# Optimization experiments

Hardware: AMD Instinct MI355X
Metric: run time of the kernel (lower is better)

The kernel has to match this reference:

```python
import jax, jax.numpy as jnp
import numpy as np

N = 100_000      # nodes
E = 1_600_000    # edges
DIN = 128
DH = 128
DOUT = 2
BN_EPS = 1e-5


def setup_inputs() -> dict:
    key = jax.random.key(0)
    ks = jax.random.split(key, 14)
    s_in = 1.0 / np.sqrt(DIN)
    s_h = 1.0 / np.sqrt(DH)
    return {
        "x": jax.random.normal(ks[0], (N, DIN), jnp.float32),
        "edge_index": jax.random.randint(ks[1], (2, E), 0, N, jnp.int32),
        "W1": jax.random.normal(ks[2], (DIN, DH), jnp.float32) * s_in,
        "b1": jnp.zeros((DH,), jnp.float32),
        "W2": jax.random.normal(ks[3], (DH, DH), jnp.float32) * s_h,
        "b2": jnp.zeros((DH,), jnp.float32),
        "W3": jax.random.normal(ks[4], (DH, DH), jnp.float32) * s_h,
        "b3": jnp.zeros((DH,), jnp.float32),
        "gamma": jnp.ones((DH,), jnp.float32),
        "beta": jnp.zeros((DH,), jnp.float32),
        "Wc": jax.random.normal(ks[5], (DH, DH), jnp.float32) * s_h,
        "bc": jnp.zeros((DH,), jnp.float32),
        "Wr": jax.random.normal(ks[6], (DH, DOUT), jnp.float32) * s_h,
        "br": jnp.zeros((DOUT,), jnp.float32),
    }


def reference(x, edge_index, W1, b1, W2, b2, W3, b3, gamma, beta, Wc, bc, Wr, br):
    src, dst = edge_index[0], edge_index[1]
    # GCN symmetric normalization with self-loops (deg includes self-loop)
    deg = jnp.zeros((N,), x.dtype).at[dst].add(1.0) + 1.0
    dinv = jax.lax.rsqrt(deg)
    coef = (dinv[src] * dinv[dst])[:, None]        # [E,1]
    self_coef = (dinv * dinv)[:, None]             # [N,1] self-loop weight

    def gcn_conv(h, W, b):
        h = h @ W                                  # [N,DH] dense transform
        agg = jnp.zeros((N, h.shape[1]), h.dtype).at[dst].add(h[src] * coef)
        return agg + h * self_coef + b

    h = jax.nn.relu(gcn_conv(x, W1, b1))
    h = jax.nn.relu(gcn_conv(h, W2, b2))   # dropout is identity at inference
    h = jax.nn.relu(gcn_conv(h, W3, b3))
    # BatchNorm1d over the node dimension (training-mode batch statistics)
    mu = h.mean(axis=0)
    var = h.var(axis=0)
    h = (h - mu) * jax.lax.rsqrt(var + BN_EPS) * gamma + beta
    h = jax.nn.relu(h @ Wc + bc)
    return h @ Wr + br
```

## Files before the change

### kernel.cpp

```cpp
#include <hip/hip_runtime.h>

#define DHC 128
#define BSHIFT 8
#define BSIZE 256

typedef __attribute__((ext_vector_type(8))) __bf16 bf16x8;
typedef __attribute__((ext_vector_type(8))) unsigned short ushort8;
typedef __attribute__((ext_vector_type(4))) float floatx4;

__device__ inline unsigned short f2bf(float f) {
    unsigned int u = __float_as_uint(f);
    return (unsigned short)((u + 0x7FFFu + ((u >> 16) & 1u)) >> 16);
}
__device__ inline float bf2f_lo(unsigned int v) { return __uint_as_float(v << 16); }
__device__ inline float bf2f_hi(unsigned int v) { return __uint_as_float(v & 0xFFFF0000u); }


__global__ __launch_bounds__(256) void bucket_hist(const int* __restrict__ dst,
                                                   int* __restrict__ bcount, int e) {
    __shared__ int h[512];
    for (int i = threadIdx.x; i < 512; i += 256) h[i] = 0;
    __syncthreads();
    int base = blockIdx.x * 4096 + threadIdx.x;
#pragma unroll
    for (int j = 0; j < 16; j++) {
        int i = base + j * 256;
        if (i < e) atomicAdd(&h[dst[i] >> BSHIFT], 1);
    }
    __syncthreads();
    for (int i = threadIdx.x; i < 512; i += 256)
        if (h[i]) atomicAdd(&bcount[i], h[i]);
}

__global__ void bucket_scan(const int* __restrict__ bcount, int* __restrict__ bbase,
                            int* __restrict__ bcur, int* __restrict__ row_ptr,
                            int nb, int n, int e) {
    __shared__ int s[512];
    int t = threadIdx.x;
    s[t] = (t < nb) ? bcount[t] : 0;
    __syncthreads();
    for (int off = 1; off < 512; off <<= 1) {
        int add = (t >= off) ? s[t - off] : 0;
        __syncthreads();
        s[t] += add;
        __syncthreads();
    }
    if (t < nb) {
        int ex = (t == 0) ? 0 : s[t - 1];
        bbase[t] = ex;
        bcur[t] = ex;
    }
    if (t == 0) {
        bbase[nb] = e;
        row_ptr[n] = e;
    }
}

__global__ __launch_bounds__(256) void bucket_scatter(const int* __restrict__ src,
                                                      const int* __restrict__ dst,
                                                      int* __restrict__ bcur,
                                                      int2* __restrict__ ebuf, int e) {
    __shared__ int h[512];
    __shared__ int rsv[512];
    for (int i = threadIdx.x; i < 512; i += 256) h[i] = 0;
    __syncthreads();
    int base = blockIdx.x * 4096 + threadIdx.x;
    int sreg[16], dreg[16];
#pragma unroll
    for (int j = 0; j < 16; j++) {
        int i = base + j * 256;
        if (i < e) {
            sreg[j] = src[i];
            dreg[j] = dst[i];
            atomicAdd(&h[dreg[j] >> BSHIFT], 1);
        } else {
            dreg[j] = -1;
        }
    }
    __syncthreads();
    for (int i = threadIdx.x; i < 512; i += 256) {
        int c = h[i];
        rsv[i] = c ? atomicAdd(&bcur[i], c) : 0;
        h[i] = 0;
    }
    __syncthreads();
#pragma unroll
    for (int j = 0; j < 16; j++) {
        if (dreg[j] >= 0) {
            int b = dreg[j] >> BSHIFT;
            int pos = rsv[b] + atomicAdd(&h[b], 1);
            ebuf[pos] = make_int2(sreg[j], dreg[j]);
        }
    }
}

__global__ __launch_bounds__(256) void bucket_build(const int2* __restrict__ ebuf,
                                                    const int* __restrict__ bbase,
                                                    int* __restrict__ row_ptr,
                                                    int* __restrict__ csr_src,
                                                    float* __restrict__ dinv,
                                                    float* __restrict__ selfc, int n) {
    __shared__ int ldeg[256];
    __shared__ int lcur[256];
    int b = blockIdx.x;
    int d0 = b << BSHIFT;
    int t = threadIdx.x;
    int beg = bbase[b], end = bbase[b + 1];
    ldeg[t] = 0;
    __syncthreads();
    for (int i = beg + t; i < end; i += 256) atomicAdd(&ldeg[ebuf[i].y - d0], 1);
    __syncthreads();
    int deg = ldeg[t];
    lcur[t] = deg;
    __syncthreads();
    for (int off = 1; off < 256; off <<= 1) {
        int add = (t >= off) ? lcur[t - off] : 0;
        __syncthreads();
        lcur[t] += add;
        __syncthreads();
    }
    int rp = beg + lcur[t] - deg;
    int node = d0 + t;
    if (node < n) {
        row_ptr[node] = rp;
        float dv = rsqrtf((float)(deg + 1));
        dinv[node] = dv;
        selfc[node] = dv * dv;
    }
    __syncthreads();
    lcur[t] = rp;
    __syncthreads();
    for (int i = beg + t; i < end; i += 256) {
        int2 p = ebuf[i];
        int pos = atomicAdd(&lcur[p.y - d0], 1);
        csr_src[pos] = p.x;
    }
}

__global__ void wconv_k(const float* __restrict__ W, unsigned short* __restrict__ WT) {
    int i = blockIdx.x * 256 + threadIdx.x;
    int nn = i >> 7, k = i & 127;
    WT[i] = f2bf(W[k * 128 + nn]);
}

template <int MODE, int AF32>
__global__ __launch_bounds__(256) void gemm_k(const void* __restrict__ Avoid,
                                              const unsigned short* __restrict__ WT,
                                              const float* __restrict__ bias,
                                              unsigned short* __restrict__ outB,
                                              float* __restrict__ outF,
                                              const float* __restrict__ Wr,
                                              const float* __restrict__ br, int n) {
    __shared__ unsigned short Ws[32 * 512];
    {
        for (int c = threadIdx.x; c < 2048; c += 256) {
            int f = c >> 6;
            int l = c & 63;
            int ks = f >> 3, ct = f & 7;
            int nn = ct * 16 + (l & 15);
            int kb = ks * 32 + (l >> 4) * 8;
            *(uint4*)(&Ws[c * 8]) = *(const uint4*)(&WT[nn * 128 + kb]);
        }
    }
    __syncthreads();
    const int wave = threadIdx.x >> 6;
    const int lane = threadIdx.x & 63;
    const int rowbase = blockIdx.x * 128 + wave * 32;
    const int m = lane & 15;
    const int kq = lane >> 4;

    floatx4 acc[2][8];
#pragma unroll
    for (int rt = 0; rt < 2; rt++)
#pragma unroll
        for (int ct = 0; ct < 8; ct++) acc[rt][ct] = (floatx4){0.f, 0.f, 0.f, 0.f};

    const int r0 = min(rowbase + m, n - 1);
    const int r1 = min(rowbase + 16 + m, n - 1);

#pragma unroll
    for (int ks = 0; ks < 4; ks++) {
        const int kb = ks * 32 + kq * 8;
        bf16x8 a0, a1;
        if (AF32) {
            const float* Af = (const float*)Avoid;
            float4 f00 = *(const float4*)(Af + (size_t)r0 * 128 + kb);
            float4 f01 = *(const float4*)(Af + (size_t)r0 * 128 + kb + 4);
            float4 f10 = *(const float4*)(Af + (size_t)r1 * 128 + kb);
            float4 f11 = *(const float4*)(Af + (size_t)r1 * 128 + kb + 4);
            ushort8 u0, u1;
            u0[0] = f2bf(f00.x); u0[1] = f2bf(f00.y); u0[2] = f2bf(f00.z); u0[3] = f2bf(f00.w);
            u0[4] = f2bf(f01.x); u0[5] = f2bf(f01.y); u0[6] = f2bf(f01.z); u0[7] = f2bf(f01.w);
            u1[0] = f2bf(f10.x); u1[1] = f2bf(f10.y); u1[2] = f2bf(f10.z); u1[3] = f2bf(f10.w);
            u1[4] = f2bf(f11.x); u1[5] = f2bf(f11.y); u1[6] = f2bf(f11.z); u1[7] = f2bf(f11.w);
            a0 = __builtin_bit_cast(bf16x8, u0);
            a1 = __builtin_bit_cast(bf16x8, u1);
        } else {
            const unsigned short* Ab = (const unsigned short*)Avoid;
            a0 = __builtin_bit_cast(bf16x8, *(const ushort8*)(Ab + (size_t)r0 * 128 + kb));
            a1 = __builtin_bit_cast(bf16x8, *(const ushort8*)(Ab + (size_t)r1 * 128 + kb));
        }
#pragma unroll
        for (int ct = 0; ct < 8; ct++) {
            bf16x8 bfr = __builtin_bit_cast(bf16x8,
                *(const ushort8*)(&Ws[(ks * 8 + ct) * 512 + lane * 8]));
            acc[0][ct] = __builtin_amdgcn_mfma_f32_16x16x32_bf16(a0, bfr, acc[0][ct], 0, 0, 0);
            acc[1][ct] = __builtin_amdgcn_mfma_f32_16x16x32_bf16(a1, bfr, acc[1][ct], 0, 0, 0);
        }
    }

    if (MODE == 0) {
#pragma unroll
        for (int rt = 0; rt < 2; rt++) {
#pragma unroll
            for (int ct = 0; ct < 8; ct++) {
                int col = ct * 16 + m;
#pragma unroll
                for (int i = 0; i < 4; i++) {
                    int r = rowbase + rt * 16 + kq * 4 + i;
                    if (r < n) outB[(size_t)r * 128 + col] = f2bf(acc[rt][ct][i]);
                }
            }
        }
    } else {
        float bcv[8], wr0[8], wr1[8];
#pragma unroll
        for (int ct = 0; ct < 8; ct++) {
            int col = ct * 16 + m;
            bcv[ct] = bias[col];
            float2 wv = ((const float2*)Wr)[col];
            wr0[ct] = wv.x;
            wr1[ct] = wv.y;
        }
        float br0 = br[0], br1 = br[1];
#pragma unroll
        for (int rt = 0; rt < 2; rt++) {
#pragma unroll
            for (int i = 0; i < 4; i++) {
                float p0 = 0.f, p1 = 0.f;
#pragma unroll
                for (int ct = 0; ct < 8; ct++) {
                    float v = fmaxf(acc[rt][ct][i] + bcv[ct], 0.f);
                    p0 = fmaf(v, wr0[ct], p0);
                    p1 = fmaf(v, wr1[ct], p1);
                }
#pragma unroll
                for (int mk = 1; mk < 16; mk <<= 1) {
                    p0 += __shfl_xor(p0, mk);
                    p1 += __shfl_xor(p1, mk);
                }
                int r = rowbase + rt * 16 + kq * 4 + i;
                if (m == 0 && r < n) ((float2*)outF)[r] = make_float2(p0 + br0, p1 + br1);
            }
        }
    }
}

__global__ __launch_bounds__(256) void agg_k(const unsigned short* __restrict__ hW,
                                             const int* __restrict__ csr,
                                             const int* __restrict__ row_ptr,
                                             const float* __restrict__ dinv,
                                             const float* __restrict__ selfc,
                                             const float* __restrict__ bias,
                                             unsigned short* __restrict__ out, int n) {
    int node = blockIdx.x * 4 + (threadIdx.x >> 6);
    int lane = threadIdx.x & 63;
    if (node >= n) return;
    int g = lane >> 4, t = lane & 15;
    int beg = row_ptr[node], end = row_ptr[node + 1];
    float dd = dinv[node];
    const uint4* h4 = (const uint4*)hW;
    float a[8];
#pragma unroll
    for (int i = 0; i < 8; i++) a[i] = 0.f;

    auto edge = [&](int e) {
        int s = csr[e];
        float c = dinv[s] * dd;
        uint4 v = h4[(size_t)s * 16 + t];
        a[0] = fmaf(c, bf2f_lo(v.x), a[0]);
        a[1] = fmaf(c, bf2f_hi(v.x), a[1]);
        a[2] = fmaf(c, bf2f_lo(v.y), a[2]);
        a[3] = fmaf(c, bf2f_hi(v.y), a[3]);
        a[4] = fmaf(c, bf2f_lo(v.z), a[4]);
        a[5] = fmaf(c, bf2f_hi(v.z), a[5]);
        a[6] = fmaf(c, bf2f_lo(v.w), a[6]);
        a[7] = fmaf(c, bf2f_hi(v.w), a[7]);
    };
    int e = beg + g;
    for (; e + 4 < end; e += 8) {
        edge(e);
        edge(e + 4);
    }
    if (e < end) edge(e);

    if (g == 0) {
        float sc = selfc[node];
        uint4 v = h4[(size_t)node * 16 + t];
        a[0] = fmaf(sc, bf2f_lo(v.x), a[0]);
        a[1] = fmaf(sc, bf2f_hi(v.x), a[1]);
        a[2] = fmaf(sc, bf2f_lo(v.y), a[2]);
        a[3] = fmaf(sc, bf2f_hi(v.y), a[3]);
        a[4] = fmaf(sc, bf2f_lo(v.z), a[4]);
        a[5] = fmaf(sc, bf2f_hi(v.z), a[5]);
        a[6] = fmaf(sc, bf2f_lo(v.w), a[6]);
        a[7] = fmaf(sc, bf2f_hi(v.w), a[7]);
    }
#pragma unroll
    for (int i = 0; i < 8; i++) {
        a[i] += __shfl_xor(a[i], 16);
        a[i] += __shfl_xor(a[i], 32);
    }
    if (g == 0) {
        float4 b0 = ((const float4*)bias)[t * 2];
        float4 b1 = ((const float4*)bias)[t * 2 + 1];
        uint4 o;
        o.x = (unsigned int)f2bf(fmaxf(a[0] + b0.x, 0.f)) |
              ((unsigned int)f2bf(fmaxf(a[1] + b0.y, 0.f)) << 16);
        o.y = (unsigned int)f2bf(fmaxf(a[2] + b0.z, 0.f)) |
              ((unsigned int)f2bf(fmaxf(a[3] + b0.w, 0.f)) << 16);
        o.z = (unsigned int)f2bf(fmaxf(a[4] + b1.x, 0.f)) |
              ((unsigned int)f2bf(fmaxf(a[5] + b1.y, 0.f)) << 16);
        o.w = (unsigned int)f2bf(fmaxf(a[6] + b1.z, 0.f)) |
              ((unsigned int)f2bf(fmaxf(a[7] + b1.w, 0.f)) << 16);
        ((uint4*)out)[(size_t)node * 16 + t] = o;
    }
}

__global__ __launch_bounds__(256) void bn_stats(const unsigned short* __restrict__ h,
                                                float* __restrict__ gsum,
                                                float* __restrict__ gsumsq, int n) {
    __shared__ float red[4][256];
    int l = threadIdx.x & 63;
    int rs = threadIdx.x >> 6;
    float s0 = 0.f, s1 = 0.f, q0 = 0.f, q1 = 0.f;
    for (int r = blockIdx.x * 4 + rs; r < n; r += gridDim.x * 4) {
        unsigned int v = *(const unsigned int*)(h + (size_t)r * 128 + l * 2);
        float a = bf2f_lo(v), b = bf2f_hi(v);
        s0 += a;
        s1 += b;
        q0 = fmaf(a, a, q0);
        q1 = fmaf(b, b, q1);
    }
    red[0][threadIdx.x] = s0;
    red[1][threadIdx.x] = s1;
    red[2][threadIdx.x] = q0;
    red[3][threadIdx.x] = q1;
    __syncthreads();
    if (threadIdx.x < 64) {
        float S0 = 0.f, S1 = 0.f, Q0 = 0.f, Q1 = 0.f;
#pragma unroll
        for (int j = 0; j < 4; j++) {
            S0 += red[0][j * 64 + l];
            S1 += red[1][j * 64 + l];
            Q0 += red[2][j * 64 + l];
            Q1 += red[3][j * 64 + l];
        }
        atomicAdd(&gsum[2 * l + 0], S0);
        atomicAdd(&gsum[2 * l + 1], S1);
        atomicAdd(&gsumsq[2 * l + 0], Q0);
        atomicAdd(&gsumsq[2 * l + 1], Q1);
    }
}

__global__ void bn_fold(const float* __restrict__ gsum, const float* __restrict__ gsumsq,
                        const float* __restrict__ gamma, const float* __restrict__ beta,
                        const float* __restrict__ Wc, const float* __restrict__ bc,
                        unsigned short* __restrict__ WcT, float* __restrict__ bcP, float invN) {
    __shared__ float scaleS[128], shiftS[128];
    int j = threadIdx.x;
    float mu = gsum[j] * invN;
    float var = gsumsq[j] * invN - mu * mu;
    float sc = gamma[j] * rsqrtf(var + 1e-5f);
    scaleS[j] = sc;
    shiftS[j] = beta[j] - mu * sc;
    __syncthreads();
    float accB = bc[j];
    for (int k = 0; k < 128; k++) {
        float w = Wc[k * 128 + j];
        WcT[j * 128 + k] = f2bf(scaleS[k] * w);
        accB = fmaf(shiftS[k], w, accB);
    }
    bcP[j] = accB;
}


extern "C" void kernel_launch(void* const* d_in, const int* in_sizes, int n_in,
                              void* d_out, int out_size, void* d_ws, size_t ws_size,
                              hipStream_t stream) {
    const float* x = (const float*)d_in[0];
    const int* ei = (const int*)d_in[1];
    const float* W1 = (const float*)d_in[2];
    const float* b1 = (const float*)d_in[3];
    const float* W2 = (const float*)d_in[4];
    const float* b2 = (const float*)d_in[5];
    const float* W3 = (const float*)d_in[6];
    const float* b3 = (const float*)d_in[7];
    const float* gamma = (const float*)d_in[8];
    const float* beta = (const float*)d_in[9];
    const float* Wc = (const float*)d_in[10];
    const float* bc = (const float*)d_in[11];
    const float* Wr = (const float*)d_in[12];
    const float* br = (const float*)d_in[13];
    float* out = (float*)d_out;

    const int N = in_sizes[0] / DHC;
    const int E = in_sizes[1] / 2;
    const int* srcIdx = ei;
    const int* dstIdx = ei + E;
    const int NB = (N + BSIZE - 1) >> BSHIFT;

    char* w = (char*)d_ws;
    size_t off = 0;
    auto alloc = [&](size_t bytes) -> void* {
        void* p = w + off;
        off += (bytes + 255) & ~(size_t)255;
        return p;
    };
    unsigned short* bufA = (unsigned short*)alloc((size_t)N * DHC * 2);
    unsigned short* bufB = (unsigned short*)alloc((size_t)N * DHC * 2);
    int2* ebuf = (int2*)alloc((size_t)E * 8);
    int* csr_src = (int*)alloc((size_t)E * 4);
    int* row_ptr = (int*)alloc((size_t)(N + 1) * 4);
    float* dinv = (float*)alloc((size_t)N * 4);
    float* selfc = (float*)alloc((size_t)N * 4);
    int* bcount = (int*)alloc(512 * 4);
    int* bbase = (int*)alloc(512 * 4);
    int* bcur = (int*)alloc(512 * 4);
    float* stats = (float*)alloc(256 * 4);
    float* gsum = stats;
    float* gsumsq = stats + 128;
    unsigned short* WT1 = (unsigned short*)alloc(16384 * 2);
    unsigned short* WT2 = (unsigned short*)alloc(16384 * 2);
    unsigned short* WT3 = (unsigned short*)alloc(16384 * 2);
    unsigned short* WcT = (unsigned short*)alloc(16384 * 2);
    float* bcP = (float*)alloc(128 * 4);
    (void)ws_size; (void)n_in; (void)out_size;

    hipMemsetAsync(bcount, 0, 512 * 4, stream);
    hipMemsetAsync(stats, 0, 256 * 4, stream);

    const int EB = (E + 4095) / 4096;
    bucket_hist<<<EB, 256, 0, stream>>>(dstIdx, bcount, E);
    bucket_scan<<<1, 512, 0, stream>>>(bcount, bbase, bcur, row_ptr, NB, N, E);
    bucket_scatter<<<EB, 256, 0, stream>>>(srcIdx, dstIdx, bcur, ebuf, E);
    bucket_build<<<NB, 256, 0, stream>>>(ebuf, bbase, row_ptr, csr_src, dinv, selfc, N);

    wconv_k<<<64, 256, 0, stream>>>(W1, WT1);
    wconv_k<<<64, 256, 0, stream>>>(W2, WT2);
    wconv_k<<<64, 256, 0, stream>>>(W3, WT3);

    const int gemmBlocks = (N + 127) / 128;
    const int aggBlocks = (N + 3) / 4;

    gemm_k<0, 1><<<gemmBlocks, 256, 0, stream>>>(x, WT1, nullptr, bufB, nullptr, nullptr, nullptr, N);
    agg_k<<<aggBlocks, 256, 0, stream>>>(bufB, csr_src, row_ptr, dinv, selfc, b1, bufA, N);
    gemm_k<0, 0><<<gemmBlocks, 256, 0, stream>>>(bufA, WT2, nullptr, bufB, nullptr, nullptr, nullptr, N);
    agg_k<<<aggBlocks, 256, 0, stream>>>(bufB, csr_src, row_ptr, dinv, selfc, b2, bufA, N);
    gemm_k<0, 0><<<gemmBlocks, 256, 0, stream>>>(bufA, WT3, nullptr, bufB, nullptr, nullptr, nullptr, N);
    agg_k<<<aggBlocks, 256, 0, stream>>>(bufB, csr_src, row_ptr, dinv, selfc, b3, bufA, N);

    bn_stats<<<256, 256, 0, stream>>>(bufA, gsum, gsumsq, N);
    bn_fold<<<1, 128, 0, stream>>>(gsum, gsumsq, gamma, beta, Wc, bc, WcT, bcP, 1.0f / (float)N);
    gemm_k<2, 0><<<gemmBlocks, 256, 0, stream>>>(bufA, WcT, bcP, nullptr, out, Wr, br, N);
}
```

Before: 500.7 us.

## Pack edge buffer, keep GEMM weights in registers, and merge small launches

Packs each bucketed edge into one 32-bit word (20-bit source, 8-bit local destination), which halves ebuf traffic in the scatter and build passes. The GEMM now loads its weight fragments directly into registers and no longer stages them through shared memory. It also sets a launch bound for two blocks per SM. Aggregation gives each of the four edge groups a contiguous chunk and unrolls by four to keep more loads in flight. The three weight conversions become one kernel and the two memsets become one, cutting launch overhead. The packing only works when node ids fit in 20 bits, and the register-held weights raise register pressure.

```diff
diff --git a/kernel.cpp b/kernel.cpp
--- a/kernel.cpp
+++ b/kernel.cpp
@@ -59,7 +59,7 @@
 __global__ __launch_bounds__(256) void bucket_scatter(const int* __restrict__ src,
                                                       const int* __restrict__ dst,
                                                       int* __restrict__ bcur,
-                                                      int2* __restrict__ ebuf, int e) {
+                                                      unsigned int* __restrict__ ebuf, int e) {
     __shared__ int h[512];
     __shared__ int rsv[512];
     for (int i = threadIdx.x; i < 512; i += 256) h[i] = 0;
@@ -89,12 +89,12 @@
         if (dreg[j] >= 0) {
             int b = dreg[j] >> BSHIFT;
             int pos = rsv[b] + atomicAdd(&h[b], 1);
-            ebuf[pos] = make_int2(sreg[j], dreg[j]);
-        }
-    }
-}
-
-__global__ __launch_bounds__(256) void bucket_build(const int2* __restrict__ ebuf,
+            ebuf[pos] = (unsigned int)sreg[j] | ((unsigned int)(dreg[j] & (BSIZE - 1)) << 20);
+        }
+    }
+}
+
+__global__ __launch_bounds__(256) void bucket_build(const unsigned int* __restrict__ ebuf,
                                                     const int* __restrict__ bbase,
                                                     int* __restrict__ row_ptr,
                                                     int* __restrict__ csr_src,
@@ -103,12 +103,11 @@
     __shared__ int ldeg[256];
     __shared__ int lcur[256];
     int b = blockIdx.x;
-    int d0 = b << BSHIFT;
     int t = threadIdx.x;
     int beg = bbase[b], end = bbase[b + 1];
     ldeg[t] = 0;
     __syncthreads();
-    for (int i = beg + t; i < end; i += 256) atomicAdd(&ldeg[ebuf[i].y - d0], 1);
+    for (int i = beg + t; i < end; i += 256) atomicAdd(&ldeg[ebuf[i] >> 20], 1);
     __syncthreads();
     int deg = ldeg[t];
     lcur[t] = deg;
@@ -120,7 +119,7 @@
         __syncthreads();
     }
     int rp = beg + lcur[t] - deg;
-    int node = d0 + t;
+    int node = (b << BSHIFT) + t;
     if (node < n) {
         row_ptr[node] = rp;
         float dv = rsqrtf((float)(deg + 1));
@@ -131,52 +130,55 @@
     lcur[t] = rp;
     __syncthreads();
     for (int i = beg + t; i < end; i += 256) {
-        int2 p = ebuf[i];
-        int pos = atomicAdd(&lcur[p.y - d0], 1);
-        csr_src[pos] = p.x;
-    }
-}
-
-__global__ void wconv_k(const float* __restrict__ W, unsigned short* __restrict__ WT) {
-    int i = blockIdx.x * 256 + threadIdx.x;
+        unsigned int p = ebuf[i];
+        int pos = atomicAdd(&lcur[p >> 20], 1);
+        csr_src[pos] = (int)(p & 0xFFFFFu);
+    }
+}
+
+__global__ void wconv3_k(const float* __restrict__ W1, const float* __restrict__ W2,
+                         const float* __restrict__ W3, unsigned short* __restrict__ WTall) {
+    int idx = blockIdx.x * 256 + threadIdx.x;
+    int wsel = idx >> 14;
+    int i = idx & 16383;
     int nn = i >> 7, k = i & 127;
-    WT[i] = f2bf(W[k * 128 + nn]);
+    const float* W = (wsel == 0) ? W1 : (wsel == 1) ? W2 : W3;
+    WTall[idx] = f2bf(W[k * 128 + nn]);
 }
 
 template <int MODE, int AF32>
-__global__ __launch_bounds__(256) void gemm_k(const void* __restrict__ Avoid,
-                                              const unsigned short* __restrict__ WT,
-                                              const float* __restrict__ bias,
-                                              unsigned short* __restrict__ outB,
-                                              float* __restrict__ outF,
-                                              const float* __restrict__ Wr,
-                                              const float* __restrict__ br, int n) {
-    __shared__ unsigned short Ws[32 * 512];
-    {
-        for (int c = threadIdx.x; c < 2048; c += 256) {
-            int f = c >> 6;
-            int l = c & 63;
-            int ks = f >> 3, ct = f & 7;
-            int nn = ct * 16 + (l & 15);
-            int kb = ks * 32 + (l >> 4) * 8;
-            *(uint4*)(&Ws[c * 8]) = *(const uint4*)(&WT[nn * 128 + kb]);
-        }
-    }
-    __syncthreads();
+__global__ __launch_bounds__(256, 2) void gemm_k(const void* __restrict__ Avoid,
+                                                 const unsigned short* __restrict__ WT,
+                                                 const float* __restrict__ bias,
+                                                 unsigned short* __restrict__ outB,
+                                                 float* __restrict__ outF,
+                                                 const float* __restrict__ Wr,
+                                                 const float* __restrict__ br, int n) {
     const int wave = threadIdx.x >> 6;
     const int lane = threadIdx.x & 63;
-    const int rowbase = blockIdx.x * 128 + wave * 32;
     const int m = lane & 15;
     const int kq = lane >> 4;
 
-    floatx4 acc[2][8];
-#pragma unroll
-    for (int rt = 0; rt < 2; rt++)
-#pragma unroll
-        for (int ct = 0; ct < 8; ct++) acc[rt][ct] = (floatx4){0.f, 0.f, 0.f, 0.f};
-
+    bf16x8 bfrag[4][8];
+#pragma unroll
+    for (int ks = 0; ks < 4; ks++) {
+        const int kb = ks * 32 + kq * 8;
+#pragma unroll
+        for (int ct = 0; ct < 8; ct++) {
+            int nn = ct * 16 + m;
+            bfrag[ks][ct] = __builtin_bit_cast(bf16x8, *(const ushort8*)(WT + nn * 128 + kb));
+        }
+    }
+
+    const int rowbase = (blockIdx.x * 4 + wave) * 32;
     const int r0 = min(rowbase + m, n - 1);
     const int r1 = min(rowbase + 16 + m, n - 1);
+
+    floatx4 acc[2][8];
+#pragma unroll
+    for (int rt = 0; rt < 2; rt++)
+#pragma unroll
+        for (int ct = 0; ct < 8; ct++) acc[rt][ct] = (floatx4){0.f, 0.f, 0.f, 0.f};
 
 #pragma unroll
     for (int ks = 0; ks < 4; ks++) {
@@ -202,10 +204,8 @@
         }
 #pragma unroll
         for (int ct = 0; ct < 8; ct++) {
-            bf16x8 bfr = __builtin_bit_cast(bf16x8,
-                *(const ushort8*)(&Ws[(ks * 8 + ct) * 512 + lane * 8]));
-            acc[0][ct] = __builtin_amdgcn_mfma_f32_16x16x32_bf16(a0, bfr, acc[0][ct], 0, 0, 0);
-            acc[1][ct] = __builtin_amdgcn_mfma_f32_16x16x32_bf16(a1, bfr, acc[1][ct], 0, 0, 0);
+            acc[0][ct] = __builtin_amdgcn_mfma_f32_16x16x32_bf16(a0, bfrag[ks][ct], acc[0][ct], 0, 0, 0);
+            acc[1][ct] = __builtin_amdgcn_mfma_f32_16x16x32_bf16(a1, bfrag[ks][ct], acc[1][ct], 0, 0, 0);
         }
     }
 
@@ -274,37 +274,52 @@
 #pragma unroll
     for (int i = 0; i < 8; i++) a[i] = 0.f;
 
-    auto edge = [&](int e) {
+    int len = end - beg;
+    int q = (len + 3) >> 2;
+    int e = beg + g * q;
+    int e1 = min(e + q, end);
+
+    for (; e + 3 < e1; e += 4) {
+        int s0 = csr[e + 0], s1 = csr[e + 1], s2 = csr[e + 2], s3 = csr[e + 3];
+        float c0 = dinv[s0] * dd, c1 = dinv[s1] * dd, c2 = dinv[s2] * dd, c3 = dinv[s3] * dd;
+        uint4 v0 = h4[(size_t)s0 * 16 + t];
+        uint4 v1 = h4[(size_t)s1 * 16 + t];
+        uint4 v2 = h4[(size_t)s2 * 16 + t];
+        uint4 v3 = h4[(size_t)s3 * 16 + t];
+        a[0] = fmaf(c0, bf2f_lo(v0.x), a[0]); a[1] = fmaf(c0, bf2f_hi(v0.x), a[1]);
+        a[2] = fmaf(c0, bf2f_lo(v0.y), a[2]); a[3] = fmaf(c0, bf2f_hi(v0.y), a[3]);
+        a[4] = fmaf(c0, bf2f_lo(v0.z), a[4]); a[5] = fmaf(c0, bf2f_hi(v0.z), a[5]);
+        a[6] = fmaf(c0, bf2f_lo(v0.w), a[6]); a[7] = fmaf(c0, bf2f_hi(v0.w), a[7]);
+        a[0] = fmaf(c1, bf2f_lo(v1.x), a[0]); a[1] = fmaf(c1, bf2f_hi(v1.x), a[1]);
+        a[2] = fmaf(c1, bf2f_lo(v1.y), a[2]); a[3] = fmaf(c1, bf2f_hi(v1.y), a[3]);
+        a[4] = fmaf(c1, bf2f_lo(v1.z), a[4]); a[5] = fmaf(c1, bf2f_hi(v1.z), a[5]);
+        a[6] = fmaf(c1, bf2f_lo(v1.w), a[6]); a[7] = fmaf(c1, bf2f_hi(v1.w), a[7]);
+        a[0] = fmaf(c2, bf2f_lo(v2.x), a[0]); a[1] = fmaf(c2, bf2f_hi(v2.x), a[1]);
+        a[2] = fmaf(c2, bf2f_lo(v2.y), a[2]); a[3] = fmaf(c2, bf2f_hi(v2.y), a[3]);
+        a[4] = fmaf(c2, bf2f_lo(v2.z), a[4]); a[5] = fmaf(c2, bf2f_hi(v2.z), a[5]);
+        a[6] = fmaf(c2, bf2f_lo(v2.w), a[6]); a[7] = fmaf(c2, bf2f_hi(v2.w), a[7]);
+        a[0] = fmaf(c3, bf2f_lo(v3.x), a[0]); a[1] = fmaf(c3, bf2f_hi(v3.x), a[1]);
+        a[2] = fmaf(c3, bf2f_lo(v3.y), a[2]); a[3] = fmaf(c3, bf2f_hi(v3.y), a[3]);
+        a[4] = fmaf(c3, bf2f_lo(v3.z), a[4]); a[5] = fmaf(c3, bf2f_hi(v3.z), a[5]);
+        a[6] = fmaf(c3, bf2f_lo(v3.w), a[6]); a[7] = fmaf(c3, bf2f_hi(v3.w), a[7]);
+    }
+    for (; e < e1; e++) {
         int s = csr[e];
         float c = dinv[s] * dd;
         uint4 v = h4[(size_t)s * 16 + t];
-        a[0] = fmaf(c, bf2f_lo(v.x), a[0]);
-        a[1] = fmaf(c, bf2f_hi(v.x), a[1]);
-        a[2] = fmaf(c, bf2f_lo(v.y), a[2]);
-        a[3] = fmaf(c, bf2f_hi(v.y), a[3]);
-        a[4] = fmaf(c, bf2f_lo(v.z), a[4]);
-        a[5] = fmaf(c, bf2f_hi(v.z), a[5]);
-        a[6] = fmaf(c, bf2f_lo(v.w), a[6]);
-        a[7] = fmaf(c, bf2f_hi(v.w), a[7]);
-    };
-    int e = beg + g;
-    for (; e + 4 < end; e += 8) {
-        edge(e);
-        edge(e + 4);
-    }
-    if (e < end) edge(e);
+        a[0] = fmaf(c, bf2f_lo(v.x), a[0]); a[1] = fmaf(c, bf2f_hi(v.x), a[1]);
+        a[2] = fmaf(c, bf2f_lo(v.y), a[2]); a[3] = fmaf(c, bf2f_hi(v.y), a[3]);
+        a[4] = fmaf(c, bf2f_lo(v.z), a[4]); a[5] = fmaf(c, bf2f_hi(v.z), a[5]);
+        a[6] = fmaf(c, bf2f_lo(v.w), a[6]); a[7] = fmaf(c, bf2f_hi(v.w), a[7]);
+    }
 
     if (g == 0) {
         float sc = selfc[node];
         uint4 v = h4[(size_t)node * 16 + t];
-        a[0] = fmaf(sc, bf2f_lo(v.x), a[0]);
-        a[1] = fmaf(sc, bf2f_hi(v.x), a[1]);
-        a[2] = fmaf(sc, bf2f_lo(v.y), a[2]);
-        a[3] = fmaf(sc, bf2f_hi(v.y), a[3]);
-        a[4] = fmaf(sc, bf2f_lo(v.z), a[4]);
-        a[5] = fmaf(sc, bf2f_hi(v.z), a[5]);
-        a[6] = fmaf(sc, bf2f_lo(v.w), a[6]);
-        a[7] = fmaf(sc, bf2f_hi(v.w), a[7]);
+        a[0] = fmaf(sc, bf2f_lo(v.x), a[0]); a[1] = fmaf(sc, bf2f_hi(v.x), a[1]);
+        a[2] = fmaf(sc, bf2f_lo(v.y), a[2]); a[3] = fmaf(sc, bf2f_hi(v.y), a[3]);
+        a[4] = fmaf(sc, bf2f_lo(v.z), a[4]); a[5] = fmaf(sc, bf2f_hi(v.z), a[5]);
+        a[6] = fmaf(sc, bf2f_lo(v.w), a[6]); a[7] = fmaf(sc, bf2f_hi(v.w), a[7]);
     }
 #pragma unroll
     for (int i = 0; i < 8; i++) {
@@ -419,26 +434,26 @@
     };
     unsigned short* bufA = (unsigned short*)alloc((size_t)N * DHC * 2);
     unsigned short* bufB = (unsigned short*)alloc((size_t)N * DHC * 2);
-    int2* ebuf = (int2*)alloc((size_t)E * 8);
+    unsigned int* ebuf = (unsigned int*)alloc((size_t)E * 4);
     int* csr_src = (int*)alloc((size_t)E * 4);
     int* row_ptr = (int*)alloc((size_t)(N + 1) * 4);
     float* dinv = (float*)alloc((size_t)N * 4);
     float* selfc = (float*)alloc((size_t)N * 4);
-    int* bcount = (int*)alloc(512 * 4);
+    int* bcount = (int*)alloc(512 * 4 + 256 * 4);
+    float* stats = (float*)(bcount + 512);
+    float* gsum = stats;
+    float* gsumsq = stats + 128;
     int* bbase = (int*)alloc(512 * 4);
     int* bcur = (int*)alloc(512 * 4);
-    float* stats = (float*)alloc(256 * 4);
-    float* gsum = stats;
-    float* gsumsq = stats + 128;
-    unsigned short* WT1 = (unsigned short*)alloc(16384 * 2);
-    unsigned short* WT2 = (unsigned short*)alloc(16384 * 2);
-    unsigned short* WT3 = (unsigned short*)alloc(16384 * 2);
+    unsigned short* WTall = (unsigned short*)alloc((size_t)3 * 16384 * 2);
+    unsigned short* WT1 = WTall;
+    unsigned short* WT2 = WTall + 16384;
+    unsigned short* WT3 = WTall + 32768;
     unsigned short* WcT = (unsigned short*)alloc(16384 * 2);
     float* bcP = (float*)alloc(128 * 4);
     (void)ws_size; (void)n_in; (void)out_size;
 
-    hipMemsetAsync(bcount, 0, 512 * 4, stream);
-    hipMemsetAsync(stats, 0, 256 * 4, stream);
+    hipMemsetAsync(bcount, 0, 512 * 4 + 256 * 4, stream);
 
     const int EB = (E + 4095) / 4096;
     bucket_hist<<<EB, 256, 0, stream>>>(dstIdx, bcount, E);
@@ -446,9 +461,7 @@
     bucket_scatter<<<EB, 256, 0, stream>>>(srcIdx, dstIdx, bcur, ebuf, E);
     bucket_build<<<NB, 256, 0, stream>>>(ebuf, bbase, row_ptr, csr_src, dinv, selfc, N);
 
-    wconv_k<<<64, 256, 0, stream>>>(W1, WT1);
-    wconv_k<<<64, 256, 0, stream>>>(W2, WT2);
-    wconv_k<<<64, 256, 0, stream>>>(W3, WT3);
+    wconv3_k<<<192, 256, 0, stream>>>(W1, W2, W3, WTall);
 
     const int gemmBlocks = (N + 127) / 128;
     const int aggBlocks = (N + 3) / 4;
```

After: 504.3 us. Within noise of the previous version (+0.7%).
